# Performance work log

Hardware: AMD Instinct MI355X
Metric: run time of the kernel (lower is better)

Reference implementation:

```python
import jax, jax.numpy as jnp
import numpy as np

HIDDEN = 256
HEADS = 4
HEAD_DIM = HIDDEN // HEADS
SCALE = HEAD_DIM ** -0.5
N1, N2 = 6000, 6000


def setup_inputs() -> dict:
    key = jax.random.key(0)
    ks = jax.random.split(key, 12)
    s = 1.0 / np.sqrt(HIDDEN)
    return {
        "kg1_emb": jax.random.normal(ks[0], (N1, HIDDEN), jnp.float32),
        "kg2_emb": jax.random.normal(ks[1], (N2, HIDDEN), jnp.float32),
        "alignment_matrix": jax.random.bernoulli(ks[2], 0.01, (N1, N2)).astype(jnp.float32),
        "Wq": jax.random.normal(ks[3], (HIDDEN, HIDDEN), jnp.float32) * s,
        "bq": jnp.zeros((HIDDEN,), jnp.float32),
        "Wk": jax.random.normal(ks[4], (HIDDEN, HIDDEN), jnp.float32) * s,
        "bk": jnp.zeros((HIDDEN,), jnp.float32),
        "Wv": jax.random.normal(ks[5], (HIDDEN, HIDDEN), jnp.float32) * s,
        "bv": jnp.zeros((HIDDEN,), jnp.float32),
        "Wo": jax.random.normal(ks[6], (HIDDEN, HIDDEN), jnp.float32) * s,
        "bo": jnp.zeros((HIDDEN,), jnp.float32),
    }


def _cross_attend(q_emb, kv_emb, align, Wq, bq, Wk, bk, Wv, bv):
    # q_emb: [Nq, H*D], kv_emb: [Nk, H*D], align: [Nq, Nk]
    Nq, Nk = q_emb.shape[0], kv_emb.shape[0]
    Q = (q_emb @ Wq.T + bq).reshape(Nq, HEADS, HEAD_DIM)
    K = (kv_emb @ Wk.T + bk).reshape(Nk, HEADS, HEAD_DIM)
    V = (kv_emb @ Wv.T + bv).reshape(Nk, HEADS, HEAD_DIM)
    # einsum('nih,mjh->nmij').mean(-1) == Q against head-mean of K (same math)
    Kbar = K.mean(axis=1)  # [Nk, D]
    scores = jnp.einsum('nid,md->nmi', Q, Kbar) * SCALE  # [Nq, Nk, HEADS]
    scores = scores * align[:, :, None]                  # multiplicative mask
    w = jax.nn.softmax(scores, axis=1)                   # over kv entities
    out = jnp.einsum('nmh,mhd->nhd', w, V)               # [Nq, HEADS, D]
    return out.reshape(Nq, HIDDEN)


def reference(kg1_emb, kg2_emb, alignment_matrix, Wq, bq, Wk, bk, Wv, bv, Wo, bo):
    kg1_from_kg2 = _cross_attend(kg1_emb, kg2_emb, alignment_matrix,
                                 Wq, bq, Wk, bk, Wv, bv)
    kg1_enhanced = kg1_emb + (kg1_from_kg2 @ Wo.T + bo)
    kg2_from_kg1 = _cross_attend(kg2_emb, kg1_emb, alignment_matrix.T,
                                 Wq, bq, Wk, bk, Wv, bv)
    kg2_enhanced = kg2_emb + (kg2_from_kg1 @ Wo.T + bo)
    return (kg1_enhanced, kg2_enhanced)
```

## Files before the change

kernel.cpp:

```cpp
#include <hip/hip_runtime.h>
#include <hip/hip_bf16.h>
#include <stdint.h>

typedef __bf16 bf16_t;
typedef __bf16 bf16x8 __attribute__((ext_vector_type(8)));
typedef __bf16 bf16x4 __attribute__((ext_vector_type(4)));
typedef float f32x4 __attribute__((ext_vector_type(4)));

#define NROW 6000
#define HID 256
#define NHEAD 4
#define HD 64
#define ATT_SCALE 0.125f
#define MTOT 12000
#define CAP 128
#define NCH16 2250000

#define CANON_BLOCKS 1024
#define SCAN_BLOCKS  ((NCH16 + 255) / 256)
#define PROJ_BLOCKS  (188 * 12)
#define CSC_BLOCKS   ((NROW * CAP) / 256)

__global__ __launch_bounds__(256)
void l1_canon_scan(const float* __restrict__ wq, const float* __restrict__ wk,
                   const float* __restrict__ wv, const float* __restrict__ wo,
                   bf16_t* __restrict__ cW,
                   const float* __restrict__ am,
                   int* __restrict__ rcur,
                   int* __restrict__ csr)
{
    if (blockIdx.x < CANON_BLOCKS) {
        int i = blockIdx.x * 256 + threadIdx.x;
        int seg = i >> 16, k = i & 65535;
        const float* s = (seg == 0) ? wq : (seg == 1) ? wk : (seg == 2) ? wv : wo;
        cW[i] = (bf16_t)s[k];
        return;
    }
    int lane = threadIdx.x & 63;
    int ch   = (blockIdx.x - CANON_BLOCKS) * 256 + threadIdx.x;
    bool oob = (ch >= NCH16);
    int che  = oob ? (NCH16 - 1) : ch;

    unsigned int nzmask = 0;
    if (!oob) {
        const uint4* p4 = (const uint4*)((const unsigned int*)am + (size_t)che * 16);
        uint4 u0 = p4[0], u1 = p4[1], u2 = p4[2], u3 = p4[3];
        unsigned int any = u0.x | u0.y | u0.z | u0.w | u1.x | u1.y | u1.z | u1.w
                         | u2.x | u2.y | u2.z | u2.w | u3.x | u3.y | u3.z | u3.w;
        if (any) {
            unsigned int w[16] = {u0.x, u0.y, u0.z, u0.w, u1.x, u1.y, u1.z, u1.w,
                                  u2.x, u2.y, u2.z, u2.w, u3.x, u3.y, u3.z, u3.w};
#pragma unroll
            for (int p = 0; p < 16; ++p)
                if (w[p]) nzmask |= 1u << p;
        }
    }
    int n  = che / 375;
    int m0 = (che - n * 375) * 16;
    int c  = __popc(nzmask);

    int p = c;
#pragma unroll
    for (int off = 1; off < 64; off <<= 1) {
        int t = __shfl_up(p, off);
        if (lane >= off) p += t;
    }
    int excl  = p - c;
    int total = __shfl(p, 63);

    int nFirst = __shfl(n, 0);
    int nLast  = __shfl(n, 63);
    unsigned long long mb = __ballot(n == nLast);
    int s0  = __ffsll(mb) - 1;
    int pS0 = __shfl(excl, s0);

    int baseB = 0;
    if (lane == s0) {
        int totalB = total - pS0;
        if (totalB > 0) baseB = atomicAdd(rcur + nLast, totalB);
    }
    baseB = __shfl(baseB, s0);
    int baseA = 0;
    if (s0 > 0) {
        if (lane == 0 && pS0 > 0) baseA = atomicAdd(rcur + nFirst, pS0);
        baseA = __shfl(baseA, 0);
    }

    int myOff = (n == nLast) ? (baseB + excl - pS0) : (baseA + excl);
    if (c) {
        int* dst = csr + (size_t)n * CAP;
        int w = 0;
#pragma unroll
        for (int pb = 0; pb < 16; ++pb) {
            if (nzmask & (1u << pb)) {
                int idx = myOff + (w++);
                if (idx < CAP) dst[idx] = m0 + pb;
            }
        }
    }
}

__global__ __launch_bounds__(256)
void l2_proj_csc(const float* __restrict__ e1, const float* __restrict__ e2,
                 const bf16_t* __restrict__ cW,
                 const float* __restrict__ bq, const float* __restrict__ bk,
                 const float* __restrict__ bv,
                 bf16_t* __restrict__ Q, bf16_t* __restrict__ Kf, bf16_t* __restrict__ V,
                 const int* __restrict__ rcnt, const int* __restrict__ csr,
                 int* __restrict__ ccur, int* __restrict__ csc)
{
    if (blockIdx.x >= PROJ_BLOCKS) {
        int tid = (blockIdx.x - PROJ_BLOCKS) * 256 + threadIdx.x;
        int n = tid >> 7, j = tid & (CAP - 1);
        if (n >= NROW) return;
        int cnt = rcnt[n]; if (cnt > CAP) cnt = CAP;
        if (j >= cnt) return;
        int m = csr[(size_t)n * CAP + j];
        int slot = atomicAdd(ccur + m, 1);
        if (slot < CAP) csc[(size_t)m * CAP + slot] = n;
        return;
    }
    int bx   = blockIdx.x;
    int m0   = (bx % 188) * 64;
    int n0   = (bx / 188) * 64;
    int wave = threadIdx.x >> 6;
    int lane = threadIdx.x & 63;
    int r16  = lane & 15;
    int quad = lane >> 4;

    int sel = n0 >> 8;
    int jb  = n0 & 255;
    const bf16_t* W = cW + (size_t)sel * HID * HID;
    const float* bias = (sel == 0) ? bq : (sel == 1) ? bk : bv;

    int arow = m0 + wave * 16 + r16;
    int rr   = arow < MTOT ? arow : MTOT - 1;
    const float* asrc = (rr < NROW) ? (e1 + (size_t)rr * HID)
                                    : (e2 + (size_t)(rr - NROW) * HID);

    f32x4 acc0 = {0,0,0,0}, acc1 = {0,0,0,0}, acc2 = {0,0,0,0}, acc3 = {0,0,0,0};
#pragma unroll
    for (int kk = 0; kk < HID; kk += 32) {
        f32x4 af0 = *(const f32x4*)(asrc + kk + quad * 8);
        f32x4 af1 = *(const f32x4*)(asrc + kk + quad * 8 + 4);
        bf16x8 a;
#pragma unroll
        for (int i = 0; i < 4; ++i) { a[i] = (bf16_t)af0[i]; a[4 + i] = (bf16_t)af1[i]; }
        const bf16_t* b0 = W + (size_t)(jb + r16) * HID + kk + quad * 8;
        bf16x8 f0 = *(const bf16x8*)(b0);
        bf16x8 f1 = *(const bf16x8*)(b0 + 16 * HID);
        bf16x8 f2 = *(const bf16x8*)(b0 + 32 * HID);
        bf16x8 f3 = *(const bf16x8*)(b0 + 48 * HID);
        acc0 = __builtin_amdgcn_mfma_f32_16x16x32_bf16(a, f0, acc0, 0, 0, 0);
        acc1 = __builtin_amdgcn_mfma_f32_16x16x32_bf16(a, f1, acc1, 0, 0, 0);
        acc2 = __builtin_amdgcn_mfma_f32_16x16x32_bf16(a, f2, acc2, 0, 0, 0);
        acc3 = __builtin_amdgcn_mfma_f32_16x16x32_bf16(a, f3, acc3, 0, 0, 0);
    }
    f32x4 accs[4] = {acc0, acc1, acc2, acc3};
    bf16_t* dst = (sel == 0) ? Q : (sel == 1) ? Kf : V;
    int rbase = m0 + wave * 16 + quad * 4;
#pragma unroll
    for (int nt = 0; nt < 4; ++nt) {
        int j = jb + nt * 16 + r16;
        float bb = bias[j];
#pragma unroll
        for (int rg = 0; rg < 4; ++rg) {
            int r = rbase + rg;
            if (r < MTOT)
                dst[(size_t)r * HID + j] = (bf16_t)(accs[nt][rg] + bb);
        }
    }
}

__global__ __launch_bounds__(256)
void kbar_vsum_kernel(const bf16_t* __restrict__ Kf, const bf16_t* __restrict__ V,
                      bf16_t* __restrict__ Kbar, float* __restrict__ Vsum)
{
    int b = blockIdx.x;
    if (b < 3000) {
        int id = b * 256 + threadIdx.x;
        int m = id >> 6, d = id & 63;
        const bf16_t* kr = Kf + (size_t)m * HID + d;
        Kbar[id] = (bf16_t)(0.25f * ((float)kr[0] + (float)kr[64] +
                                     (float)kr[128] + (float)kr[192]));
    } else {
        int idx = b - 3000;
        int g = idx / 24;
        int seg = idx - g * 24;
        int j = threadIdx.x;
        const bf16_t* base = V + ((size_t)(g * NROW + seg * 250)) * HID + j;
        float s = 0.f;
        for (int m = 0; m < 250; ++m) s += (float)base[(size_t)m * HID];
        atomicAdd(Vsum + g * HID + j, s);
    }
}

__global__ __launch_bounds__(256)
void attn_kernel(const bf16_t* __restrict__ Q, const bf16_t* __restrict__ Kbar,
                 const bf16_t* __restrict__ V, const float* __restrict__ Vsum,
                 const int* __restrict__ rcnt, const int* __restrict__ ccnt,
                 const int* __restrict__ csr, const int* __restrict__ csc,
                 bf16_t* __restrict__ att)
{
    __shared__ __align__(16) bf16_t qsb[HID];
    __shared__ int   ml[CAP];
    __shared__ float sc[CAP * 5];
    __shared__ float w0s[NHEAD];
    __shared__ float red[4 * HID];

    int dir = blockIdx.y;
    int n   = blockIdx.x;
    int t   = threadIdx.x;
    int wave = t >> 6, lane = t & 63;

    size_t qrow = (size_t)(dir ? NROW + n : n);
    const bf16_t* kb_base = Kbar + (dir ? 0 : (size_t)NROW * HD);
    const bf16_t* v_base  = V    + (dir ? 0 : (size_t)NROW * HID);
    const float*  vs      = Vsum + (dir ? 0 : HID);
    const int*    lst     = (dir ? csc : csr) + (size_t)n * CAP;
    int cnt = (dir ? ccnt : rcnt)[n];
    if (cnt > CAP) cnt = CAP;

    qsb[t] = Q[qrow * HID + t];
    for (int j = t; j < cnt; j += 256) ml[j] = lst[j];
    __syncthreads();

    int m16  = lane & 15;
    int quad = lane >> 4;

    {
        bf16x8 b0, b1;
        if (m16 < NHEAD) {
            b0 = *(const bf16x8*)(qsb + m16 * HD + 0  + quad * 8);
            b1 = *(const bf16x8*)(qsb + m16 * HD + 32 + quad * 8);
        } else {
            b0 = (bf16x8)(bf16_t)0.f;
            b1 = (bf16x8)(bf16_t)0.f;
        }
        for (int jt = wave; jt * 16 < cnt; jt += 4) {
            int j  = jt * 16 + m16;
            int jj = j < cnt ? j : cnt - 1;
            int row = ml[jj];
            const bf16_t* ap = kb_base + (size_t)row * HD + quad * 8;
            bf16x8 a0 = *(const bf16x8*)(ap);
            bf16x8 a1 = *(const bf16x8*)(ap + 32);
            f32x4 acc = {0, 0, 0, 0};
            acc = __builtin_amdgcn_mfma_f32_16x16x32_bf16(a0, b0, acc, 0, 0, 0);
            acc = __builtin_amdgcn_mfma_f32_16x16x32_bf16(a1, b1, acc, 0, 0, 0);
            if (m16 < NHEAD) {
#pragma unroll
                for (int rg = 0; rg < 4; ++rg) {
                    int jw = jt * 16 + quad * 4 + rg;
                    if (jw < cnt) sc[jw * 5 + m16] = acc[rg] * ATT_SCALE;
                }
            }
        }
    }
    __syncthreads();

    {
        int head = wave;
        float M = 0.0f;
        for (int j = lane; j < cnt; j += 64) M = fmaxf(M, sc[j * 5 + head]);
        for (int off = 32; off; off >>= 1) M = fmaxf(M, __shfl_xor(M, off));
        float e0 = __expf(-M);
        float e[2]; int k = 0;
        float S = 0.f;
        for (int j = lane; j < cnt; j += 64, ++k) { e[k] = __expf(sc[j * 5 + head] - M); S += e[k]; }
        for (int off = 32; off; off >>= 1) S += __shfl_xor(S, off);
        float Z = S + (float)(NROW - cnt) * e0;
        float invZ = 1.0f / Z;
        k = 0;
        for (int j = lane; j < cnt; j += 64, ++k) sc[j * 5 + head] = (e[k] - e0) * invZ;
        if (lane == 0) w0s[head] = e0 * invZ;
    }
    __syncthreads();

    int h3 = lane >> 4;
    int dq = lane & 15;
    int colb = h3 * HD + dq * 4;
    float a0 = 0.f, a1 = 0.f, a2 = 0.f, a3 = 0.f;
    {
        int j = wave;
        for (; j + 4 < cnt; j += 8) {
            int   m0 = ml[j];            int   m1 = ml[j + 4];
            float c0 = sc[j * 5 + h3];   float c1 = sc[(j + 4) * 5 + h3];
            bf16x4 r0 = *(const bf16x4*)(v_base + (size_t)m0 * HID + colb);
            bf16x4 r1 = *(const bf16x4*)(v_base + (size_t)m1 * HID + colb);
            a0 += c0 * (float)r0[0] + c1 * (float)r1[0];
            a1 += c0 * (float)r0[1] + c1 * (float)r1[1];
            a2 += c0 * (float)r0[2] + c1 * (float)r1[2];
            a3 += c0 * (float)r0[3] + c1 * (float)r1[3];
        }
        if (j < cnt) {
            int   m0 = ml[j];
            float c0 = sc[j * 5 + h3];
            bf16x4 r0 = *(const bf16x4*)(v_base + (size_t)m0 * HID + colb);
            a0 += c0 * (float)r0[0];
            a1 += c0 * (float)r0[1];
            a2 += c0 * (float)r0[2];
            a3 += c0 * (float)r0[3];
        }
    }
    red[wave * 256 + colb + 0] = a0;
    red[wave * 256 + colb + 1] = a1;
    red[wave * 256 + colb + 2] = a2;
    red[wave * 256 + colb + 3] = a3;
    __syncthreads();
    float tot = red[t] + red[256 + t] + red[512 + t] + red[768 + t]
              + w0s[t >> 6] * vs[t];
    att[qrow * HID + t] = (bf16_t)tot;
}

__global__ __launch_bounds__(256)
void proj_out_kernel(const bf16_t* __restrict__ att, const bf16_t* __restrict__ wo,
                     const float* __restrict__ bo,
                     const float* __restrict__ e1, const float* __restrict__ e2,
                     float* __restrict__ out)
{
    int m0   = blockIdx.x * 64;
    int n0   = blockIdx.y * 64;
    int wave = threadIdx.x >> 6;
    int lane = threadIdx.x & 63;
    int r16  = lane & 15;
    int quad = lane >> 4;

    int arow = m0 + wave * 16 + r16;
    int rr   = arow < MTOT ? arow : MTOT - 1;
    const bf16_t* asrc = att + (size_t)rr * HID;

    f32x4 acc0 = {0,0,0,0}, acc1 = {0,0,0,0}, acc2 = {0,0,0,0}, acc3 = {0,0,0,0};
#pragma unroll
    for (int kk = 0; kk < HID; kk += 32) {
        bf16x8 a = *(const bf16x8*)(asrc + kk + quad * 8);
        const bf16_t* b0 = wo + (size_t)(n0 + r16) * HID + kk + quad * 8;
        bf16x8 f0 = *(const bf16x8*)(b0);
        bf16x8 f1 = *(const bf16x8*)(b0 + 16 * HID);
        bf16x8 f2 = *(const bf16x8*)(b0 + 32 * HID);
        bf16x8 f3 = *(const bf16x8*)(b0 + 48 * HID);
        acc0 = __builtin_amdgcn_mfma_f32_16x16x32_bf16(a, f0, acc0, 0, 0, 0);
        acc1 = __builtin_amdgcn_mfma_f32_16x16x32_bf16(a, f1, acc1, 0, 0, 0);
        acc2 = __builtin_amdgcn_mfma_f32_16x16x32_bf16(a, f2, acc2, 0, 0, 0);
        acc3 = __builtin_amdgcn_mfma_f32_16x16x32_bf16(a, f3, acc3, 0, 0, 0);
    }
    f32x4 accs[4] = {acc0, acc1, acc2, acc3};
    int rbase = m0 + wave * 16 + quad * 4;
#pragma unroll
    for (int nt = 0; nt < 4; ++nt) {
        int j = n0 + nt * 16 + r16;
        float bb = bo[j];
#pragma unroll
        for (int rg = 0; rg < 4; ++rg) {
            int r = rbase + rg;
            if (r < MTOT) {
                const float* emb = (r < NROW) ? (e1 + (size_t)r * HID)
                                              : (e2 + (size_t)(r - NROW) * HID);
                float v = accs[nt][rg] + bb + emb[j];
                out[(size_t)r * HID + j] = v;
            }
        }
    }
}

extern "C" void kernel_launch(void* const* d_in, const int* in_sizes, int n_in,
                              void* d_out, int out_size, void* d_ws, size_t ws_size,
                              hipStream_t stream)
{
    const float* e1 = (const float*)d_in[0];
    const float* e2 = (const float*)d_in[1];
    const float* am = (const float*)d_in[2];
    const float* wq = (const float*)d_in[3];
    const float* bq = (const float*)d_in[4];
    const float* wk = (const float*)d_in[5];
    const float* bk = (const float*)d_in[6];
    const float* wv = (const float*)d_in[7];
    const float* bv = (const float*)d_in[8];
    const float* wo = (const float*)d_in[9];
    const float* bo = (const float*)d_in[10];
    float* out = (float*)d_out;

    size_t off = 0;
    char* base = (char*)d_ws;
    auto alloc = [&](size_t bytes) -> void* {
        void* p = base + off;
        off += (bytes + 255) & ~(size_t)255;
        return p;
    };
    bf16_t* Q    = (bf16_t*)alloc((size_t)MTOT * HID * 2);
    bf16_t* Kf   = (bf16_t*)alloc((size_t)MTOT * HID * 2);
    bf16_t* V    = (bf16_t*)alloc((size_t)MTOT * HID * 2);
    bf16_t* Kbar = (bf16_t*)alloc((size_t)MTOT * HD * 2);
    bf16_t* att  = (bf16_t*)alloc((size_t)MTOT * HID * 2);
    bf16_t* cW   = (bf16_t*)alloc((size_t)4 * HID * HID * 2);
    int*    csr  = (int*)   alloc((size_t)NROW * CAP * 4);
    int*    csc  = (int*)   alloc((size_t)NROW * CAP * 4);
    int*    rcur = (int*)   alloc(NROW * 4);
    int*    ccur = (int*)   alloc(NROW * 4);
    float*  Vsum = (float*) alloc(2 * HID * 4);

    size_t zero_bytes = (size_t)((char*)Vsum - (char*)rcur) + 2 * HID * 4;
    hipMemsetAsync(rcur, 0, zero_bytes, stream);

    l1_canon_scan<<<CANON_BLOCKS + SCAN_BLOCKS, 256, 0, stream>>>(
        wq, wk, wv, wo, cW, am, rcur, csr);

    l2_proj_csc<<<PROJ_BLOCKS + CSC_BLOCKS, 256, 0, stream>>>(
        e1, e2, cW, bq, bk, bv, Q, Kf, V, rcur, csr, ccur, csc);

    kbar_vsum_kernel<<<3048, 256, 0, stream>>>(Kf, V, Kbar, Vsum);

    attn_kernel<<<dim3(NROW, 2), 256, 0, stream>>>(
        Q, Kbar, V, Vsum, rcur, ccur, csr, csc, att);

    proj_out_kernel<<<dim3(188, 4), 256, 0, stream>>>(
        att, cW + 3 * HID * HID, bo, e1, e2, out);
}
```

Before: 373.4 us.

## Fuse projections into scan kernel, stage weights in LDS, merge CSC into aux kernel

Drops the separate weight-canonicalisation pass. Each projection block now converts its 64-row fp32 weight slice to bf16 directly into padded LDS, and the QKV projection runs in the same launch as the alignment scan. The CSC build is folded into the Kbar/Vsum kernel, cutting the launch count from five to four. The attention V-accumulation loop is unrolled to four gathered rows per iteration. In exchange, every projection block repeats the weight conversion and uses extra LDS, which may reduce occupancy.

```diff
diff --git a/kernel.cpp b/kernel.cpp
--- a/kernel.cpp
+++ b/kernel.cpp
@@ -16,28 +16,91 @@
 #define CAP 128
 #define NCH16 2250000
 
-#define CANON_BLOCKS 1024
 #define SCAN_BLOCKS  ((NCH16 + 255) / 256)
 #define PROJ_BLOCKS  (188 * 12)
 #define CSC_BLOCKS   ((NROW * CAP) / 256)
+#define WSTR 264
 
 __global__ __launch_bounds__(256)
-void l1_canon_scan(const float* __restrict__ wq, const float* __restrict__ wk,
-                   const float* __restrict__ wv, const float* __restrict__ wo,
-                   bf16_t* __restrict__ cW,
-                   const float* __restrict__ am,
-                   int* __restrict__ rcur,
-                   int* __restrict__ csr)
+void k1_proj_scan(const float* __restrict__ e1, const float* __restrict__ e2,
+                  const float* __restrict__ wq, const float* __restrict__ wk,
+                  const float* __restrict__ wv,
+                  const float* __restrict__ bq, const float* __restrict__ bk,
+                  const float* __restrict__ bv,
+                  bf16_t* __restrict__ Q, bf16_t* __restrict__ Kf, bf16_t* __restrict__ V,
+                  const float* __restrict__ am,
+                  int* __restrict__ rcur,
+                  int* __restrict__ csr)
 {
-    if (blockIdx.x < CANON_BLOCKS) {
-        int i = blockIdx.x * 256 + threadIdx.x;
-        int seg = i >> 16, k = i & 65535;
-        const float* s = (seg == 0) ? wq : (seg == 1) ? wk : (seg == 2) ? wv : wo;
-        cW[i] = (bf16_t)s[k];
+    __shared__ bf16_t lds_w[64 * WSTR];
+
+    if (blockIdx.x < PROJ_BLOCKS) {
+        int bx   = blockIdx.x;
+        int m0   = (bx % 188) * 64;
+        int n0   = (bx / 188) * 64;
+        int wave = threadIdx.x >> 6;
+        int lane = threadIdx.x & 63;
+        int r16  = lane & 15;
+        int quad = lane >> 4;
+
+        int sel = n0 >> 8;
+        int jb  = n0 & 255;
+        const float* wsrc = (sel == 0) ? wq : (sel == 1) ? wk : wv;
+        const float* bias = (sel == 0) ? bq : (sel == 1) ? bk : bv;
+
+        for (int i = threadIdx.x; i < 64 * 64; i += 256) {
+            int row = i >> 6;
+            int kq  = (i & 63) * 4;
+            f32x4 w4 = *(const f32x4*)(wsrc + (size_t)(jb + row) * HID + kq);
+            bf16x4 b4;
+#pragma unroll
+            for (int z = 0; z < 4; ++z) b4[z] = (bf16_t)w4[z];
+            *(bf16x4*)(&lds_w[row * WSTR + kq]) = b4;
+        }
+        __syncthreads();
+
+        int arow = m0 + wave * 16 + r16;
+        int rr   = arow < MTOT ? arow : MTOT - 1;
+        const float* asrc = (rr < NROW) ? (e1 + (size_t)rr * HID)
+                                        : (e2 + (size_t)(rr - NROW) * HID);
+
+        f32x4 acc0 = {0,0,0,0}, acc1 = {0,0,0,0}, acc2 = {0,0,0,0}, acc3 = {0,0,0,0};
+#pragma unroll
+        for (int kk = 0; kk < HID; kk += 32) {
+            f32x4 af0 = *(const f32x4*)(asrc + kk + quad * 8);
+            f32x4 af1 = *(const f32x4*)(asrc + kk + quad * 8 + 4);
+            bf16x8 a;
+#pragma unroll
+            for (int i = 0; i < 4; ++i) { a[i] = (bf16_t)af0[i]; a[4 + i] = (bf16_t)af1[i]; }
+            const bf16_t* b0 = lds_w + (size_t)r16 * WSTR + kk + quad * 8;
+            bf16x8 f0 = *(const bf16x8*)(b0);
+            bf16x8 f1 = *(const bf16x8*)(b0 + 16 * WSTR);
+            bf16x8 f2 = *(const bf16x8*)(b0 + 32 * WSTR);
+            bf16x8 f3 = *(const bf16x8*)(b0 + 48 * WSTR);
+            acc0 = __builtin_amdgcn_mfma_f32_16x16x32_bf16(a, f0, acc0, 0, 0, 0);
+            acc1 = __builtin_amdgcn_mfma_f32_16x16x32_bf16(a, f1, acc1, 0, 0, 0);
+            acc2 = __builtin_amdgcn_mfma_f32_16x16x32_bf16(a, f2, acc2, 0, 0, 0);
+            acc3 = __builtin_amdgcn_mfma_f32_16x16x32_bf16(a, f3, acc3, 0, 0, 0);
+        }
+        f32x4 accs[4] = {acc0, acc1, acc2, acc3};
+        bf16_t* dst = (sel == 0) ? Q : (sel == 1) ? Kf : V;
+        int rbase = m0 + wave * 16 + quad * 4;
+#pragma unroll
+        for (int nt = 0; nt < 4; ++nt) {
+            int j = jb + nt * 16 + r16;
+            float bb = bias[j];
+#pragma unroll
+            for (int rg = 0; rg < 4; ++rg) {
+                int r = rbase + rg;
+                if (r < MTOT)
+                    dst[(size_t)r * HID + j] = (bf16_t)(accs[nt][rg] + bb);
+            }
+        }
         return;
     }
+
     int lane = threadIdx.x & 63;
-    int ch   = (blockIdx.x - CANON_BLOCKS) * 256 + threadIdx.x;
+    int ch   = (blockIdx.x - PROJ_BLOCKS) * 256 + threadIdx.x;
     bool oob = (ch >= NCH16);
     int che  = oob ? (NCH16 - 1) : ch;
 
@@ -101,80 +164,10 @@
 }
 
 __global__ __launch_bounds__(256)
-void l2_proj_csc(const float* __restrict__ e1, const float* __restrict__ e2,
-                 const bf16_t* __restrict__ cW,
-                 const float* __restrict__ bq, const float* __restrict__ bk,
-                 const float* __restrict__ bv,
-                 bf16_t* __restrict__ Q, bf16_t* __restrict__ Kf, bf16_t* __restrict__ V,
-                 const int* __restrict__ rcnt, const int* __restrict__ csr,
-                 int* __restrict__ ccur, int* __restrict__ csc)
-{
-    if (blockIdx.x >= PROJ_BLOCKS) {
-        int tid = (blockIdx.x - PROJ_BLOCKS) * 256 + threadIdx.x;
-        int n = tid >> 7, j = tid & (CAP - 1);
-        if (n >= NROW) return;
-        int cnt = rcnt[n]; if (cnt > CAP) cnt = CAP;
-        if (j >= cnt) return;
-        int m = csr[(size_t)n * CAP + j];
-        int slot = atomicAdd(ccur + m, 1);
-        if (slot < CAP) csc[(size_t)m * CAP + slot] = n;
-        return;
-    }
-    int bx   = blockIdx.x;
-    int m0   = (bx % 188) * 64;
-    int n0   = (bx / 188) * 64;
-    int wave = threadIdx.x >> 6;
-    int lane = threadIdx.x & 63;
-    int r16  = lane & 15;
-    int quad = lane >> 4;
-
-    int sel = n0 >> 8;
-    int jb  = n0 & 255;
-    const bf16_t* W = cW + (size_t)sel * HID * HID;
-    const float* bias = (sel == 0) ? bq : (sel == 1) ? bk : bv;
-
-    int arow = m0 + wave * 16 + r16;
-    int rr   = arow < MTOT ? arow : MTOT - 1;
-    const float* asrc = (rr < NROW) ? (e1 + (size_t)rr * HID)
-                                    : (e2 + (size_t)(rr - NROW) * HID);
-
-    f32x4 acc0 = {0,0,0,0}, acc1 = {0,0,0,0}, acc2 = {0,0,0,0}, acc3 = {0,0,0,0};
-#pragma unroll
-    for (int kk = 0; kk < HID; kk += 32) {
-        f32x4 af0 = *(const f32x4*)(asrc + kk + quad * 8);
-        f32x4 af1 = *(const f32x4*)(asrc + kk + quad * 8 + 4);
-        bf16x8 a;
-#pragma unroll
-        for (int i = 0; i < 4; ++i) { a[i] = (bf16_t)af0[i]; a[4 + i] = (bf16_t)af1[i]; }
-        const bf16_t* b0 = W + (size_t)(jb + r16) * HID + kk + quad * 8;
-        bf16x8 f0 = *(const bf16x8*)(b0);
-        bf16x8 f1 = *(const bf16x8*)(b0 + 16 * HID);
-        bf16x8 f2 = *(const bf16x8*)(b0 + 32 * HID);
-        bf16x8 f3 = *(const bf16x8*)(b0 + 48 * HID);
-        acc0 = __builtin_amdgcn_mfma_f32_16x16x32_bf16(a, f0, acc0, 0, 0, 0);
-        acc1 = __builtin_amdgcn_mfma_f32_16x16x32_bf16(a, f1, acc1, 0, 0, 0);
-        acc2 = __builtin_amdgcn_mfma_f32_16x16x32_bf16(a, f2, acc2, 0, 0, 0);
-        acc3 = __builtin_amdgcn_mfma_f32_16x16x32_bf16(a, f3, acc3, 0, 0, 0);
-    }
-    f32x4 accs[4] = {acc0, acc1, acc2, acc3};
-    bf16_t* dst = (sel == 0) ? Q : (sel == 1) ? Kf : V;
-    int rbase = m0 + wave * 16 + quad * 4;
-#pragma unroll
-    for (int nt = 0; nt < 4; ++nt) {
-        int j = jb + nt * 16 + r16;
-        float bb = bias[j];
-#pragma unroll
-        for (int rg = 0; rg < 4; ++rg) {
-            int r = rbase + rg;
-            if (r < MTOT)
-                dst[(size_t)r * HID + j] = (bf16_t)(accs[nt][rg] + bb);
-        }
-    }
-}
-
-__global__ __launch_bounds__(256)
-void kbar_vsum_kernel(const bf16_t* __restrict__ Kf, const bf16_t* __restrict__ V,
-                      bf16_t* __restrict__ Kbar, float* __restrict__ Vsum)
+void k2_aux(const bf16_t* __restrict__ Kf, const bf16_t* __restrict__ V,
+            bf16_t* __restrict__ Kbar, float* __restrict__ Vsum,
+            const int* __restrict__ rcnt, const int* __restrict__ csr,
+            int* __restrict__ ccur, int* __restrict__ csc)
 {
     int b = blockIdx.x;
     if (b < 3000) {
@@ -183,7 +176,7 @@
         const bf16_t* kr = Kf + (size_t)m * HID + d;
         Kbar[id] = (bf16_t)(0.25f * ((float)kr[0] + (float)kr[64] +
                                      (float)kr[128] + (float)kr[192]));
-    } else {
+    } else if (b < 3048) {
         int idx = b - 3000;
         int g = idx / 24;
         int seg = idx - g * 24;
@@ -192,6 +185,15 @@
         float s = 0.f;
         for (int m = 0; m < 250; ++m) s += (float)base[(size_t)m * HID];
         atomicAdd(Vsum + g * HID + j, s);
+    } else {
+        int tid = (b - 3048) * 256 + threadIdx.x;
+        int n = tid >> 7, j = tid & (CAP - 1);
+        if (n >= NROW) return;
+        int cnt = rcnt[n]; if (cnt > CAP) cnt = CAP;
+        if (j >= cnt) return;
+        int m = csr[(size_t)n * CAP + j];
+        int slot = atomicAdd(ccur + m, 1);
+        if (slot < CAP) csc[(size_t)m * CAP + slot] = n;
     }
 }
 
@@ -282,17 +284,21 @@
     float a0 = 0.f, a1 = 0.f, a2 = 0.f, a3 = 0.f;
     {
         int j = wave;
-        for (; j + 4 < cnt; j += 8) {
+        for (; j + 12 < cnt; j += 16) {
             int   m0 = ml[j];            int   m1 = ml[j + 4];
+            int   m2 = ml[j + 8];        int   m3 = ml[j + 12];
             float c0 = sc[j * 5 + h3];   float c1 = sc[(j + 4) * 5 + h3];
+            float c2 = sc[(j + 8) * 5 + h3]; float c3 = sc[(j + 12) * 5 + h3];
             bf16x4 r0 = *(const bf16x4*)(v_base + (size_t)m0 * HID + colb);
             bf16x4 r1 = *(const bf16x4*)(v_base + (size_t)m1 * HID + colb);
-            a0 += c0 * (float)r0[0] + c1 * (float)r1[0];
-            a1 += c0 * (float)r0[1] + c1 * (float)r1[1];
-            a2 += c0 * (float)r0[2] + c1 * (float)r1[2];
-            a3 += c0 * (float)r0[3] + c1 * (float)r1[3];
-        }
-        if (j < cnt) {
+            bf16x4 r2 = *(const bf16x4*)(v_base + (size_t)m2 * HID + colb);
+            bf16x4 r3 = *(const bf16x4*)(v_base + (size_t)m3 * HID + colb);
+            a0 += c0 * (float)r0[0] + c1 * (float)r1[0] + c2 * (float)r2[0] + c3 * (float)r3[0];
+            a1 += c0 * (float)r0[1] + c1 * (float)r1[1] + c2 * (float)r2[1] + c3 * (float)r3[1];
+            a2 += c0 * (float)r0[2] + c1 * (float)r1[2] + c2 * (float)r2[2] + c3 * (float)r3[2];
+            a3 += c0 * (float)r0[3] + c1 * (float)r1[3] + c2 * (float)r2[3] + c3 * (float)r3[3];
+        }
+        for (; j < cnt; j += 4) {
             int   m0 = ml[j];
             float c0 = sc[j * 5 + h3];
             bf16x4 r0 = *(const bf16x4*)(v_base + (size_t)m0 * HID + colb);
@@ -313,11 +319,13 @@
 }
 
 __global__ __launch_bounds__(256)
-void proj_out_kernel(const bf16_t* __restrict__ att, const bf16_t* __restrict__ wo,
+void proj_out_kernel(const bf16_t* __restrict__ att, const float* __restrict__ wo,
                      const float* __restrict__ bo,
                      const float* __restrict__ e1, const float* __restrict__ e2,
                      float* __restrict__ out)
 {
+    __shared__ bf16_t lds_w[64 * WSTR];
+
     int m0   = blockIdx.x * 64;
     int n0   = blockIdx.y * 64;
     int wave = threadIdx.x >> 6;
@@ -325,6 +333,17 @@
     int r16  = lane & 15;
     int quad = lane >> 4;
 
+    for (int i = threadIdx.x; i < 64 * 64; i += 256) {
+        int row = i >> 6;
+        int kq  = (i & 63) * 4;
+        f32x4 w4 = *(const f32x4*)(wo + (size_t)(n0 + row) * HID + kq);
+        bf16x4 b4;
+#pragma unroll
+        for (int z = 0; z < 4; ++z) b4[z] = (bf16_t)w4[z];
+        *(bf16x4*)(&lds_w[row * WSTR + kq]) = b4;
+    }
+    __syncthreads();
+
     int arow = m0 + wave * 16 + r16;
     int rr   = arow < MTOT ? arow : MTOT - 1;
     const bf16_t* asrc = att + (size_t)rr * HID;
@@ -333,11 +352,11 @@
 #pragma unroll
     for (int kk = 0; kk < HID; kk += 32) {
         bf16x8 a = *(const bf16x8*)(asrc + kk + quad * 8);
-        const bf16_t* b0 = wo + (size_t)(n0 + r16) * HID + kk + quad * 8;
+        const bf16_t* b0 = lds_w + (size_t)r16 * WSTR + kk + quad * 8;
         bf16x8 f0 = *(const bf16x8*)(b0);
-        bf16x8 f1 = *(const bf16x8*)(b0 + 16 * HID);
-        bf16x8 f2 = *(const bf16x8*)(b0 + 32 * HID);
-        bf16x8 f3 = *(const bf16x8*)(b0 + 48 * HID);
+        bf16x8 f1 = *(const bf16x8*)(b0 + 16 * WSTR);
+        bf16x8 f2 = *(const bf16x8*)(b0 + 32 * WSTR);
+        bf16x8 f3 = *(const bf16x8*)(b0 + 48 * WSTR);
         acc0 = __builtin_amdgcn_mfma_f32_16x16x32_bf16(a, f0, acc0, 0, 0, 0);
         acc1 = __builtin_amdgcn_mfma_f32_16x16x32_bf16(a, f1, acc1, 0, 0, 0);
         acc2 = __builtin_amdgcn_mfma_f32_16x16x32_bf16(a, f2, acc2, 0, 0, 0);
@@ -391,7 +410,6 @@
     bf16_t* V    = (bf16_t*)alloc((size_t)MTOT * HID * 2);
     bf16_t* Kbar = (bf16_t*)alloc((size_t)MTOT * HD * 2);
     bf16_t* att  = (bf16_t*)alloc((size_t)MTOT * HID * 2);
-    bf16_t* cW   = (bf16_t*)alloc((size_t)4 * HID * HID * 2);
     int*    csr  = (int*)   alloc((size_t)NROW * CAP * 4);
     int*    csc  = (int*)   alloc((size_t)NROW * CAP * 4);
     int*    rcur = (int*)   alloc(NROW * 4);
@@ -401,17 +419,13 @@
     size_t zero_bytes = (size_t)((char*)Vsum - (char*)rcur) + 2 * HID * 4;
     hipMemsetAsync(rcur, 0, zero_bytes, stream);
 
-    l1_canon_scan<<<CANON_BLOCKS + SCAN_BLOCKS, 256, 0, stream>>>(
-        wq, wk, wv, wo, cW, am, rcur, csr);
-
-    l2_proj_csc<<<PROJ_BLOCKS + CSC_BLOCKS, 256, 0, stream>>>(
-        e1, e2, cW, bq, bk, bv, Q, Kf, V, rcur, csr, ccur, csc);
-
-    kbar_vsum_kernel<<<3048, 256, 0, stream>>>(Kf, V, Kbar, Vsum);
+    k1_proj_scan<<<PROJ_BLOCKS + SCAN_BLOCKS, 256, 0, stream>>>(
+        e1, e2, wq, wk, wv, bq, bk, bv, Q, Kf, V, am, rcur, csr);
+
+    k2_aux<<<6048, 256, 0, stream>>>(Kf, V, Kbar, Vsum, rcur, csr, ccur, csc);
 
     attn_kernel<<<dim3(NROW, 2), 256, 0, stream>>>(
         Q, Kbar, V, Vsum, rcur, ccur, csr, csc, att);
 
-    proj_out_kernel<<<dim3(188, 4), 256, 0, stream>>>(
-        att, cW + 3 * HID * HID, bo, e1, e2, out);
+    proj_out_kernel<<<dim3(188, 4), 256, 0, stream>>>(att, wo, bo, e1, e2, out);
 }
```

New measurement: 356.2 us. -4.6%, faster.

## Restructure kernel stages: fold memset, co-schedule projection with mask scan, unroll V gather

Applied to the files above, without the earlier changes.

The hipMemsetAsync is replaced by zeroing blocks inside the weight-canonicalisation kernel. The QKV projection now shares a launch with the alignment-matrix scan, and the CSC build moves into the Kbar/Vsum kernel, so the bandwidth-bound scan overlaps with MFMA work. The attention V-gather loop is unrolled from two to four rows per iteration for more memory-level parallelism. Together these remove one launch and rebalance work across stages, at the cost of mixing unlike workloads in one grid.

```diff
diff --git a/kernel.cpp b/kernel.cpp
--- a/kernel.cpp
+++ b/kernel.cpp
@@ -17,17 +17,16 @@
 #define NCH16 2250000
 
 #define CANON_BLOCKS 1024
+#define ZERO_INTS    12544
+#define ZERO_BLOCKS  49
 #define SCAN_BLOCKS  ((NCH16 + 255) / 256)
 #define PROJ_BLOCKS  (188 * 12)
 #define CSC_BLOCKS   ((NROW * CAP) / 256)
 
 __global__ __launch_bounds__(256)
-void l1_canon_scan(const float* __restrict__ wq, const float* __restrict__ wk,
+void k0_canon_zero(const float* __restrict__ wq, const float* __restrict__ wk,
                    const float* __restrict__ wv, const float* __restrict__ wo,
-                   bf16_t* __restrict__ cW,
-                   const float* __restrict__ am,
-                   int* __restrict__ rcur,
-                   int* __restrict__ csr)
+                   bf16_t* __restrict__ cW, int* __restrict__ zbase)
 {
     if (blockIdx.x < CANON_BLOCKS) {
         int i = blockIdx.x * 256 + threadIdx.x;
@@ -36,8 +35,76 @@
         cW[i] = (bf16_t)s[k];
         return;
     }
+    int i = (blockIdx.x - CANON_BLOCKS) * 256 + threadIdx.x;
+    if (i < ZERO_INTS) zbase[i] = 0;
+}
+
+__global__ __launch_bounds__(256)
+void k1_proj_scan(const float* __restrict__ e1, const float* __restrict__ e2,
+                  const bf16_t* __restrict__ cW,
+                  const float* __restrict__ bq, const float* __restrict__ bk,
+                  const float* __restrict__ bv,
+                  bf16_t* __restrict__ Q, bf16_t* __restrict__ Kf, bf16_t* __restrict__ V,
+                  const float* __restrict__ am,
+                  int* __restrict__ rcur,
+                  int* __restrict__ csr)
+{
+    if (blockIdx.x < PROJ_BLOCKS) {
+        int bx   = blockIdx.x;
+        int m0   = (bx % 188) * 64;
+        int n0   = (bx / 188) * 64;
+        int wave = threadIdx.x >> 6;
+        int lane = threadIdx.x & 63;
+        int r16  = lane & 15;
+        int quad = lane >> 4;
+
+        int sel = n0 >> 8;
+        int jb  = n0 & 255;
+        const bf16_t* W = cW + (size_t)sel * HID * HID;
+        const float* bias = (sel == 0) ? bq : (sel == 1) ? bk : bv;
+
+        int arow = m0 + wave * 16 + r16;
+        int rr   = arow < MTOT ? arow : MTOT - 1;
+        const float* asrc = (rr < NROW) ? (e1 + (size_t)rr * HID)
+                                        : (e2 + (size_t)(rr - NROW) * HID);
+
+        f32x4 acc0 = {0,0,0,0}, acc1 = {0,0,0,0}, acc2 = {0,0,0,0}, acc3 = {0,0,0,0};
+#pragma unroll
+        for (int kk = 0; kk < HID; kk += 32) {
+            f32x4 af0 = *(const f32x4*)(asrc + kk + quad * 8);
+            f32x4 af1 = *(const f32x4*)(asrc + kk + quad * 8 + 4);
+            bf16x8 a;
+#pragma unroll
+            for (int i = 0; i < 4; ++i) { a[i] = (bf16_t)af0[i]; a[4 + i] = (bf16_t)af1[i]; }
+            const bf16_t* b0 = W + (size_t)(jb + r16) * HID + kk + quad * 8;
+            bf16x8 f0 = *(const bf16x8*)(b0);
+            bf16x8 f1 = *(const bf16x8*)(b0 + 16 * HID);
+            bf16x8 f2 = *(const bf16x8*)(b0 + 32 * HID);
+            bf16x8 f3 = *(const bf16x8*)(b0 + 48 * HID);
+            acc0 = __builtin_amdgcn_mfma_f32_16x16x32_bf16(a, f0, acc0, 0, 0, 0);
+            acc1 = __builtin_amdgcn_mfma_f32_16x16x32_bf16(a, f1, acc1, 0, 0, 0);
+            acc2 = __builtin_amdgcn_mfma_f32_16x16x32_bf16(a, f2, acc2, 0, 0, 0);
+            acc3 = __builtin_amdgcn_mfma_f32_16x16x32_bf16(a, f3, acc3, 0, 0, 0);
+        }
+        f32x4 accs[4] = {acc0, acc1, acc2, acc3};
+        bf16_t* dst = (sel == 0) ? Q : (sel == 1) ? Kf : V;
+        int rbase = m0 + wave * 16 + quad * 4;
+#pragma unroll
+        for (int nt = 0; nt < 4; ++nt) {
+            int j = jb + nt * 16 + r16;
+            float bb = bias[j];
+#pragma unroll
+            for (int rg = 0; rg < 4; ++rg) {
+                int r = rbase + rg;
+                if (r < MTOT)
+                    dst[(size_t)r * HID + j] = (bf16_t)(accs[nt][rg] + bb);
+            }
+        }
+        return;
+    }
+
     int lane = threadIdx.x & 63;
-    int ch   = (blockIdx.x - CANON_BLOCKS) * 256 + threadIdx.x;
+    int ch   = (blockIdx.x - PROJ_BLOCKS) * 256 + threadIdx.x;
     bool oob = (ch >= NCH16);
     int che  = oob ? (NCH16 - 1) : ch;
 
@@ -101,80 +168,10 @@
 }
 
 __global__ __launch_bounds__(256)
-void l2_proj_csc(const float* __restrict__ e1, const float* __restrict__ e2,
-                 const bf16_t* __restrict__ cW,
-                 const float* __restrict__ bq, const float* __restrict__ bk,
-                 const float* __restrict__ bv,
-                 bf16_t* __restrict__ Q, bf16_t* __restrict__ Kf, bf16_t* __restrict__ V,
-                 const int* __restrict__ rcnt, const int* __restrict__ csr,
-                 int* __restrict__ ccur, int* __restrict__ csc)
-{
-    if (blockIdx.x >= PROJ_BLOCKS) {
-        int tid = (blockIdx.x - PROJ_BLOCKS) * 256 + threadIdx.x;
-        int n = tid >> 7, j = tid & (CAP - 1);
-        if (n >= NROW) return;
-        int cnt = rcnt[n]; if (cnt > CAP) cnt = CAP;
-        if (j >= cnt) return;
-        int m = csr[(size_t)n * CAP + j];
-        int slot = atomicAdd(ccur + m, 1);
-        if (slot < CAP) csc[(size_t)m * CAP + slot] = n;
-        return;
-    }
-    int bx   = blockIdx.x;
-    int m0   = (bx % 188) * 64;
-    int n0   = (bx / 188) * 64;
-    int wave = threadIdx.x >> 6;
-    int lane = threadIdx.x & 63;
-    int r16  = lane & 15;
-    int quad = lane >> 4;
-
-    int sel = n0 >> 8;
-    int jb  = n0 & 255;
-    const bf16_t* W = cW + (size_t)sel * HID * HID;
-    const float* bias = (sel == 0) ? bq : (sel == 1) ? bk : bv;
-
-    int arow = m0 + wave * 16 + r16;
-    int rr   = arow < MTOT ? arow : MTOT - 1;
-    const float* asrc = (rr < NROW) ? (e1 + (size_t)rr * HID)
-                                    : (e2 + (size_t)(rr - NROW) * HID);
-
-    f32x4 acc0 = {0,0,0,0}, acc1 = {0,0,0,0}, acc2 = {0,0,0,0}, acc3 = {0,0,0,0};
-#pragma unroll
-    for (int kk = 0; kk < HID; kk += 32) {
-        f32x4 af0 = *(const f32x4*)(asrc + kk + quad * 8);
-        f32x4 af1 = *(const f32x4*)(asrc + kk + quad * 8 + 4);
-        bf16x8 a;
-#pragma unroll
-        for (int i = 0; i < 4; ++i) { a[i] = (bf16_t)af0[i]; a[4 + i] = (bf16_t)af1[i]; }
-        const bf16_t* b0 = W + (size_t)(jb + r16) * HID + kk + quad * 8;
-        bf16x8 f0 = *(const bf16x8*)(b0);
-        bf16x8 f1 = *(const bf16x8*)(b0 + 16 * HID);
-        bf16x8 f2 = *(const bf16x8*)(b0 + 32 * HID);
-        bf16x8 f3 = *(const bf16x8*)(b0 + 48 * HID);
-        acc0 = __builtin_amdgcn_mfma_f32_16x16x32_bf16(a, f0, acc0, 0, 0, 0);
-        acc1 = __builtin_amdgcn_mfma_f32_16x16x32_bf16(a, f1, acc1, 0, 0, 0);
-        acc2 = __builtin_amdgcn_mfma_f32_16x16x32_bf16(a, f2, acc2, 0, 0, 0);
-        acc3 = __builtin_amdgcn_mfma_f32_16x16x32_bf16(a, f3, acc3, 0, 0, 0);
-    }
-    f32x4 accs[4] = {acc0, acc1, acc2, acc3};
-    bf16_t* dst = (sel == 0) ? Q : (sel == 1) ? Kf : V;
-    int rbase = m0 + wave * 16 + quad * 4;
-#pragma unroll
-    for (int nt = 0; nt < 4; ++nt) {
-        int j = jb + nt * 16 + r16;
-        float bb = bias[j];
-#pragma unroll
-        for (int rg = 0; rg < 4; ++rg) {
-            int r = rbase + rg;
-            if (r < MTOT)
-                dst[(size_t)r * HID + j] = (bf16_t)(accs[nt][rg] + bb);
-        }
-    }
-}
-
-__global__ __launch_bounds__(256)
-void kbar_vsum_kernel(const bf16_t* __restrict__ Kf, const bf16_t* __restrict__ V,
-                      bf16_t* __restrict__ Kbar, float* __restrict__ Vsum)
+void k2_aux(const bf16_t* __restrict__ Kf, const bf16_t* __restrict__ V,
+            bf16_t* __restrict__ Kbar, float* __restrict__ Vsum,
+            const int* __restrict__ rcnt, const int* __restrict__ csr,
+            int* __restrict__ ccur, int* __restrict__ csc)
 {
     int b = blockIdx.x;
     if (b < 3000) {
@@ -183,7 +180,7 @@
         const bf16_t* kr = Kf + (size_t)m * HID + d;
         Kbar[id] = (bf16_t)(0.25f * ((float)kr[0] + (float)kr[64] +
                                      (float)kr[128] + (float)kr[192]));
-    } else {
+    } else if (b < 3048) {
         int idx = b - 3000;
         int g = idx / 24;
         int seg = idx - g * 24;
@@ -192,6 +189,15 @@
         float s = 0.f;
         for (int m = 0; m < 250; ++m) s += (float)base[(size_t)m * HID];
         atomicAdd(Vsum + g * HID + j, s);
+    } else {
+        int tid = (b - 3048) * 256 + threadIdx.x;
+        int n = tid >> 7, j = tid & (CAP - 1);
+        if (n >= NROW) return;
+        int cnt = rcnt[n]; if (cnt > CAP) cnt = CAP;
+        if (j >= cnt) return;
+        int m = csr[(size_t)n * CAP + j];
+        int slot = atomicAdd(ccur + m, 1);
+        if (slot < CAP) csc[(size_t)m * CAP + slot] = n;
     }
 }
 
@@ -282,17 +288,21 @@
     float a0 = 0.f, a1 = 0.f, a2 = 0.f, a3 = 0.f;
     {
         int j = wave;
-        for (; j + 4 < cnt; j += 8) {
+        for (; j + 12 < cnt; j += 16) {
             int   m0 = ml[j];            int   m1 = ml[j + 4];
+            int   m2 = ml[j + 8];        int   m3 = ml[j + 12];
             float c0 = sc[j * 5 + h3];   float c1 = sc[(j + 4) * 5 + h3];
+            float c2 = sc[(j + 8) * 5 + h3]; float c3 = sc[(j + 12) * 5 + h3];
             bf16x4 r0 = *(const bf16x4*)(v_base + (size_t)m0 * HID + colb);
             bf16x4 r1 = *(const bf16x4*)(v_base + (size_t)m1 * HID + colb);
-            a0 += c0 * (float)r0[0] + c1 * (float)r1[0];
-            a1 += c0 * (float)r0[1] + c1 * (float)r1[1];
-            a2 += c0 * (float)r0[2] + c1 * (float)r1[2];
-            a3 += c0 * (float)r0[3] + c1 * (float)r1[3];
-        }
-        if (j < cnt) {
+            bf16x4 r2 = *(const bf16x4*)(v_base + (size_t)m2 * HID + colb);
+            bf16x4 r3 = *(const bf16x4*)(v_base + (size_t)m3 * HID + colb);
+            a0 += c0 * (float)r0[0] + c1 * (float)r1[0] + c2 * (float)r2[0] + c3 * (float)r3[0];
+            a1 += c0 * (float)r0[1] + c1 * (float)r1[1] + c2 * (float)r2[1] + c3 * (float)r3[1];
+            a2 += c0 * (float)r0[2] + c1 * (float)r1[2] + c2 * (float)r2[2] + c3 * (float)r3[2];
+            a3 += c0 * (float)r0[3] + c1 * (float)r1[3] + c2 * (float)r2[3] + c3 * (float)r3[3];
+        }
+        for (; j < cnt; j += 4) {
             int   m0 = ml[j];
             float c0 = sc[j * 5 + h3];
             bf16x4 r0 = *(const bf16x4*)(v_base + (size_t)m0 * HID + colb);
@@ -397,20 +407,18 @@
     int*    rcur = (int*)   alloc(NROW * 4);
     int*    ccur = (int*)   alloc(NROW * 4);
     float*  Vsum = (float*) alloc(2 * HID * 4);
-
-    size_t zero_bytes = (size_t)((char*)Vsum - (char*)rcur) + 2 * HID * 4;
-    hipMemsetAsync(rcur, 0, zero_bytes, stream);
-
-    l1_canon_scan<<<CANON_BLOCKS + SCAN_BLOCKS, 256, 0, stream>>>(
-        wq, wk, wv, wo, cW, am, rcur, csr);
-
-    l2_proj_csc<<<PROJ_BLOCKS + CSC_BLOCKS, 256, 0, stream>>>(
-        e1, e2, cW, bq, bk, bv, Q, Kf, V, rcur, csr, ccur, csc);
-
-    kbar_vsum_kernel<<<3048, 256, 0, stream>>>(Kf, V, Kbar, Vsum);
+    (void)Vsum;
+
+    k0_canon_zero<<<CANON_BLOCKS + ZERO_BLOCKS, 256, 0, stream>>>(
+        wq, wk, wv, wo, cW, rcur);
+
+    k1_proj_scan<<<PROJ_BLOCKS + SCAN_BLOCKS, 256, 0, stream>>>(
+        e1, e2, cW, bq, bk, bv, Q, Kf, V, am, rcur, csr);
+
+    k2_aux<<<6048, 256, 0, stream>>>(Kf, V, Kbar, (float*)Vsum, rcur, csr, ccur, csc);
 
     attn_kernel<<<dim3(NROW, 2), 256, 0, stream>>>(
-        Q, Kbar, V, Vsum, rcur, ccur, csr, csc, att);
+        Q, Kbar, V, (float*)Vsum, rcur, ccur, csr, csc, att);
 
     proj_out_kernel<<<dim3(188, 4), 256, 0, stream>>>(
         att, cW + 3 * HID * HID, bo, e1, e2, out);
```

New measurement: 373.3 us. Within noise of the previous version (-0.0%).
